# Kernel optimization log

Hardware: AMD Instinct MI355X
Metric: run time of the kernel (lower is better)

Reference implementation:

```python
import jax, jax.numpy as jnp
import numpy as np


def setup_inputs() -> dict:
    key = jax.random.key(0)
    k1, k2, k3, k4 = jax.random.split(key, 4)
    N, S, F, UNITS = 50000, 32, 128, 128
    x = jax.random.normal(k1, (N, F), dtype=jnp.float32)
    neigh_x = jax.random.normal(k2, (N, S, F), dtype=jnp.float32)
    kernel_self = jax.random.normal(k3, (F, UNITS), dtype=jnp.float32) * 0.05
    kernel_neigh = jax.random.normal(k4, (F, UNITS), dtype=jnp.float32) * 0.05
    bias = jnp.zeros((2 * UNITS,), dtype=jnp.float32)
    return {"x": x, "neigh_x": neigh_x, "kernel_self": kernel_self,
            "kernel_neigh": kernel_neigh, "bias": bias}


def reference(x, neigh_x, kernel_self, kernel_neigh, bias):
    # neigh_x: [N, S, F]. Original transposes to [N, F, S] and applies
    # tf.raw_ops.NthElement with n = S//2 + S%2 (n-th smallest, 0-indexed)
    # along the last (neighbor) axis. Equivalent: sort along neighbor axis
    # of the untransposed tensor and take index n.
    S = neigh_x.shape[1]
    n = S // 2 + S % 2
    med = jnp.sort(neigh_x, axis=1)[:, n, :]  # [N, F]
    out = jnp.concatenate([x @ kernel_self, med @ kernel_neigh], axis=1)  # [N, 2*units] (concat=True)
    out = out + bias
    return jax.nn.relu(out)
```

## Files before the change

### kernel.cpp

```cpp
#include <hip/hip_runtime.h>

namespace {

typedef float f32x2 __attribute__((ext_vector_type(2)));
typedef float f32x4 __attribute__((ext_vector_type(4)));

constexpr int S   = 32;
constexpr int F   = 128;
constexpr int BR  = 32;
constexpr int TPB = 256;

struct CEPair { int a, b; };

constexpr int batcher_count16() {
  int n = 16, cnt = 0;
  for (int p = 1; p < n; p <<= 1)
    for (int k = p; k >= 1; k >>= 1)
      for (int j = k % p; j + k < n; j += 2 * k)
        for (int i = 0; i < k && i + j + k < n; ++i)
          if ((i + j) / (2 * p) == (i + j + k) / (2 * p))
            ++cnt;
  return cnt;
}
constexpr int NCE = batcher_count16();

struct Net16 { CEPair ce[NCE]; };

constexpr Net16 make_net16() {
  Net16 net{};
  int n = 16, c = 0;
  for (int p = 1; p < n; p <<= 1)
    for (int k = p; k >= 1; k >>= 1)
      for (int j = k % p; j + k < n; j += 2 * k)
        for (int i = 0; i < k && i + j + k < n; ++i)
          if ((i + j) / (2 * p) == (i + j + k) / (2 * p))
            net.ce[c++] = CEPair{i + j, i + j + k};
  return net;
}
constexpr Net16 NET16 = make_net16();

__device__ __forceinline__ f32x2 min2(f32x2 a, f32x2 b) {
  f32x2 r; r.x = fminf(a.x, b.x); r.y = fminf(a.y, b.y); return r;
}
__device__ __forceinline__ f32x2 max2(f32x2 a, f32x2 b) {
  f32x2 r; r.x = fmaxf(a.x, b.x); r.y = fmaxf(a.y, b.y); return r;
}

template<int T>
__device__ __forceinline__ void sort16(f32x2 (&v)[16]) {
  if constexpr (T < NCE) {
    constexpr int a = NET16.ce[T].a;
    constexpr int b = NET16.ce[T].b;
    f32x2 x = v[a], y = v[b];
    v[a] = min2(x, y);
    v[b] = max2(x, y);
    sort16<T + 1>(v);
  }
}

__device__ __forceinline__ void issue_row(const float* __restrict__ neigh,
                                          const float* __restrict__ x,
                                          int row, int lane,
                                          f32x2 (&A)[16], f32x2 (&B)[16],
                                          f32x2& xv)
{
    const f32x2* nb = (const f32x2*)(neigh + (size_t)row * (S * F)) + lane;
#pragma unroll
    for (int s = 0; s < 16; ++s)
        A[s] = __builtin_nontemporal_load(nb + (size_t)s * 64);
#pragma unroll
    for (int s = 0; s < 16; ++s)
        B[s] = __builtin_nontemporal_load(nb + (size_t)(s + 16) * 64);
    xv = *((const f32x2*)(x + (size_t)row * F) + lane);
}

__device__ __forceinline__ void select_store(f32x2 (&A)[16], f32x2 (&B)[16],
                                             f32x2 xv,
                                             float* __restrict__ msrow,
                                             float* __restrict__ xsrow,
                                             int lane)
{
    sort16<0>(A);
    sort16<0>(B);
#pragma unroll
    for (int q = 0; q < 16; ++q) A[q] = max2(A[q], B[15 - q]);
#pragma unroll
    for (int st = 8; st >= 1; st >>= 1)
#pragma unroll
        for (int q = 0; q < st; ++q) A[q] = min2(A[q], A[q + st]);
    ((f32x2*)msrow)[lane] = A[0];
    ((f32x2*)xsrow)[lane] = xv;
}

__global__ __launch_bounds__(TPB, 3) void fused_median_gemm(
    const float* __restrict__ x,
    const float* __restrict__ neigh,
    const float* __restrict__ Ks,
    const float* __restrict__ Kn,
    const float* __restrict__ bias,
    float* __restrict__ out,
    int N)
{
    __shared__ __align__(16) float xs[4][8][F];
    __shared__ __align__(16) float ms[4][8][F];

    const int tid  = threadIdx.x;
    const int wv   = tid >> 6;
    const int lane = tid & 63;
    const int row0 = blockIdx.x * BR + wv * 8;

    const int rmax = N - 1;
    auto rw = [&](int rl) { int r = row0 + rl; return r > rmax ? rmax : r; };

    {
        f32x2 A0[16], B0[16], A1[16], B1[16];
        f32x2 x0, x1;

        issue_row(neigh, x, rw(0), lane, A0, B0, x0);
#pragma unroll
        for (int p = 0; p < 4; ++p) {
            issue_row(neigh, x, rw(2 * p + 1), lane, A1, B1, x1);
            select_store(A0, B0, x0, &ms[wv][2 * p][0], &xs[wv][2 * p][0], lane);
            if (p < 3)
                issue_row(neigh, x, rw(2 * p + 2), lane, A0, B0, x0);
            select_store(A1, B1, x1, &ms[wv][2 * p + 1][0], &xs[wv][2 * p + 1][0], lane);
        }
    }

    asm volatile("s_waitcnt lgkmcnt(0)" ::: "memory");

    const bool self_half = (lane < 32);
    const float* __restrict__ W = self_half ? Ks : Kn;
    const int wcol = (lane * 4) & 127;
    const float* lin = self_half ? &xs[wv][0][0] : &ms[wv][0][0];

    f32x4 acc[8];
#pragma unroll
    for (int r = 0; r < 8; ++r) acc[r] = f32x4{0.f, 0.f, 0.f, 0.f};

#pragma unroll 4
    for (int k4 = 0; k4 < 32; ++k4) {
        f32x4 wv4[4];
#pragma unroll
        for (int dk = 0; dk < 4; ++dk)
            wv4[dk] = *(const f32x4*)&W[(k4 * 4 + dk) * 128 + wcol];

        f32x4 xr[8];
#pragma unroll
        for (int r = 0; r < 8; ++r)
            xr[r] = *(const f32x4*)&lin[r * F + k4 * 4];

#pragma unroll
        for (int r = 0; r < 8; ++r) {
#pragma unroll
            for (int dk = 0; dk < 4; ++dk) {
                const float s = xr[r][dk];
                acc[r].x = fmaf(s, wv4[dk].x, acc[r].x);
                acc[r].y = fmaf(s, wv4[dk].y, acc[r].y);
                acc[r].z = fmaf(s, wv4[dk].z, acc[r].z);
                acc[r].w = fmaf(s, wv4[dk].w, acc[r].w);
            }
        }
    }

    const f32x4 bv = *(const f32x4*)&bias[lane * 4];
#pragma unroll
    for (int r = 0; r < 8; ++r) {
        const int row = rw(r);
        f32x4 o;
        o.x = fmaxf(acc[r].x + bv.x, 0.f);
        o.y = fmaxf(acc[r].y + bv.y, 0.f);
        o.z = fmaxf(acc[r].z + bv.z, 0.f);
        o.w = fmaxf(acc[r].w + bv.w, 0.f);
        __builtin_nontemporal_store(o, (f32x4*)&out[(size_t)row * 256 + lane * 4]);
    }
}

}

extern "C" void kernel_launch(void* const* d_in, const int* in_sizes, int n_in,
                              void* d_out, int out_size, void* d_ws, size_t ws_size,
                              hipStream_t stream) {
    const float* x     = (const float*)d_in[0];
    const float* neigh = (const float*)d_in[1];
    const float* Ks    = (const float*)d_in[2];
    const float* Kn    = (const float*)d_in[3];
    const float* bias  = (const float*)d_in[4];
    float* out = (float*)d_out;

    const int N = in_sizes[0] / F;
    const int grid = (N + BR - 1) / BR;
    hipLaunchKernelGGL(fused_median_gemm, dim3(grid), dim3(TPB), 0, stream,
                       x, neigh, Ks, Kn, bias, out, N);
}
```

Before: 183.6 us.

## Replace FP32 FMA GEMM with bf16 MFMA using pre-swizzled weight fragments

The median and self features are now stored to shared memory as bf16. The dense projection uses 16x16x32 bf16 MFMA instructions instead of scalar FP32 FMAs. A small pre-kernel converts both weight matrices to bf16 and lays them out in MFMA B-fragment order in the workspace. This cuts ALU work and LDS footprint in the GEMM phase, but it lowers precision to bf16. It also adds a second launch, and output stores become scalar per-column writes from half the lanes.

New measurement: 192.9 us. +5.0%, slower.

```diff
diff --git a/kernel.cpp b/kernel.cpp
--- a/kernel.cpp
+++ b/kernel.cpp
@@ -2,8 +2,10 @@
 
 namespace {
 
-typedef float f32x2 __attribute__((ext_vector_type(2)));
-typedef float f32x4 __attribute__((ext_vector_type(4)));
+typedef float  f32x2  __attribute__((ext_vector_type(2)));
+typedef float  f32x4  __attribute__((ext_vector_type(4)));
+typedef short  bf16x8 __attribute__((ext_vector_type(8)));
+typedef unsigned short u16;
 
 constexpr int S   = 32;
 constexpr int F   = 128;
@@ -58,6 +60,11 @@
   }
 }
 
+__device__ __forceinline__ unsigned f2bf(float f) {
+  unsigned u = __builtin_bit_cast(unsigned, f);
+  return (u + 0x7FFFu + ((u >> 16) & 1u)) >> 16;
+}
+
 __device__ __forceinline__ void issue_row(const float* __restrict__ neigh,
                                           const float* __restrict__ x,
                                           int row, int lane,
@@ -76,8 +83,8 @@
 
 __device__ __forceinline__ void select_store(f32x2 (&A)[16], f32x2 (&B)[16],
                                              f32x2 xv,
-                                             float* __restrict__ msrow,
-                                             float* __restrict__ xsrow,
+                                             u16* __restrict__ msrow,
+                                             u16* __restrict__ xsrow,
                                              int lane)
 {
     sort16<0>(A);
@@ -88,21 +95,43 @@
     for (int st = 8; st >= 1; st >>= 1)
 #pragma unroll
         for (int q = 0; q < st; ++q) A[q] = min2(A[q], A[q + st]);
-    ((f32x2*)msrow)[lane] = A[0];
-    ((f32x2*)xsrow)[lane] = xv;
+    ((unsigned*)msrow)[lane] = f2bf(A[0].x) | (f2bf(A[0].y) << 16);
+    ((unsigned*)xsrow)[lane] = f2bf(xv.x)   | (f2bf(xv.y)   << 16);
+}
+
+__global__ void convert_weights(const float* __restrict__ Ks,
+                                const float* __restrict__ Kn,
+                                u16* __restrict__ wsb)
+{
+    const int t  = blockIdx.x * 256 + threadIdx.x;
+    const int c  = t >> 8;
+    const int kk = (t >> 6) & 3;
+    const int l  = t & 63;
+    const int n  = c * 16 + (l & 15);
+    const int kb = kk * 32 + (l >> 4) * 8;
+    const float* __restrict__ W = (n < 128) ? Ks : Kn;
+    const int nn = n & 127;
+
+    u16 tmp[8];
+#pragma unroll
+    for (int j = 0; j < 8; ++j)
+        tmp[j] = (u16)f2bf(W[(size_t)(kb + j) * 128 + nn]);
+
+    u16* dst = wsb + (size_t)(c * 4 + kk) * 512 + (size_t)l * 8;
+#pragma unroll
+    for (int j = 0; j < 8; ++j) dst[j] = tmp[j];
 }
 
 __global__ __launch_bounds__(TPB, 3) void fused_median_gemm(
     const float* __restrict__ x,
     const float* __restrict__ neigh,
-    const float* __restrict__ Ks,
-    const float* __restrict__ Kn,
+    const u16*   __restrict__ wfrag,
     const float* __restrict__ bias,
     float* __restrict__ out,
     int N)
 {
-    __shared__ __align__(16) float xs[4][8][F];
-    __shared__ __align__(16) float ms[4][8][F];
+    __shared__ __align__(16) u16 xs[4][8][F];
+    __shared__ __align__(16) u16 ms[4][8][F];
 
     const int tid  = threadIdx.x;
     const int wv   = tid >> 6;
@@ -129,50 +158,40 @@
 
     asm volatile("s_waitcnt lgkmcnt(0)" ::: "memory");
 
-    const bool self_half = (lane < 32);
-    const float* __restrict__ W = self_half ? Ks : Kn;
-    const int wcol = (lane * 4) & 127;
-    const float* lin = self_half ? &xs[wv][0][0] : &ms[wv][0][0];
-
-    f32x4 acc[8];
-#pragma unroll
-    for (int r = 0; r < 8; ++r) acc[r] = f32x4{0.f, 0.f, 0.f, 0.f};
+    const int arow = lane & 7;
+    const int ag   = lane >> 4;
+
+    bf16x8 ax[4], am[4];
+#pragma unroll
+    for (int kk = 0; kk < 4; ++kk) {
+        ax[kk] = *(const bf16x8*)&xs[wv][arow][kk * 32 + ag * 8];
+        am[kk] = *(const bf16x8*)&ms[wv][arow][kk * 32 + ag * 8];
+    }
+
+    const bf16x8* __restrict__ wsf = (const bf16x8*)wfrag;
+    const int dcol = lane & 15;
+    const int drow = (lane >> 4) * 4;
 
 #pragma unroll 4
-    for (int k4 = 0; k4 < 32; ++k4) {
-        f32x4 wv4[4];
-#pragma unroll
-        for (int dk = 0; dk < 4; ++dk)
-            wv4[dk] = *(const f32x4*)&W[(k4 * 4 + dk) * 128 + wcol];
-
-        f32x4 xr[8];
-#pragma unroll
-        for (int r = 0; r < 8; ++r)
-            xr[r] = *(const f32x4*)&lin[r * F + k4 * 4];
-
-#pragma unroll
-        for (int r = 0; r < 8; ++r) {
-#pragma unroll
-            for (int dk = 0; dk < 4; ++dk) {
-                const float s = xr[r][dk];
-                acc[r].x = fmaf(s, wv4[dk].x, acc[r].x);
-                acc[r].y = fmaf(s, wv4[dk].y, acc[r].y);
-                acc[r].z = fmaf(s, wv4[dk].z, acc[r].z);
-                acc[r].w = fmaf(s, wv4[dk].w, acc[r].w);
+    for (int c = 0; c < 16; ++c) {
+        f32x4 acc = f32x4{0.f, 0.f, 0.f, 0.f};
+#pragma unroll
+        for (int kk = 0; kk < 4; ++kk) {
+            const bf16x8 b = wsf[(c * 4 + kk) * 64 + lane];
+            acc = __builtin_amdgcn_mfma_f32_16x16x32_bf16(
+                      (c < 8) ? ax[kk] : am[kk], b, acc, 0, 0, 0);
+        }
+        const int col = c * 16 + dcol;
+        const float bb = bias[col];
+        if (lane < 32) {
+#pragma unroll
+            for (int reg = 0; reg < 4; ++reg) {
+                int row = row0 + drow + reg;
+                if (row > rmax) row = rmax;
+                const float o = fmaxf(acc[reg] + bb, 0.f);
+                __builtin_nontemporal_store(o, &out[(size_t)row * 256 + col]);
             }
         }
-    }
-
-    const f32x4 bv = *(const f32x4*)&bias[lane * 4];
-#pragma unroll
-    for (int r = 0; r < 8; ++r) {
-        const int row = rw(r);
-        f32x4 o;
-        o.x = fmaxf(acc[r].x + bv.x, 0.f);
-        o.y = fmaxf(acc[r].y + bv.y, 0.f);
-        o.z = fmaxf(acc[r].z + bv.z, 0.f);
-        o.w = fmaxf(acc[r].w + bv.w, 0.f);
-        __builtin_nontemporal_store(o, (f32x4*)&out[(size_t)row * 256 + lane * 4]);
     }
 }
 
@@ -187,9 +206,14 @@
     const float* Kn    = (const float*)d_in[3];
     const float* bias  = (const float*)d_in[4];
     float* out = (float*)d_out;
+    u16*   wsb = (u16*)d_ws;
 
     const int N = in_sizes[0] / F;
+
+    hipLaunchKernelGGL(convert_weights, dim3(16), dim3(256), 0, stream,
+                       Ks, Kn, wsb);
+
     const int grid = (N + BR - 1) / BR;
     hipLaunchKernelGGL(fused_median_gemm, dim3(grid), dim3(TPB), 0, stream,
-                       x, neigh, Ks, Kn, bias, out, N);
-}
+                       x, neigh, wsb, bias, out, N);
+}
```
